# Optimization experiments

Measured on AMD Instinct MI355X. Metric: run time of the kernel, lower is better.

Reference implementation:

```python
import jax, jax.numpy as jnp
import numpy as np

H = 128; L = 4; B = 128; NPG = 32
N = B * NPG; E = B * NPG * NPG
NFREQ = 10; DIS = 2 * 3 * NFREQ; EIN = 2 * H + 9 + DIS  # 325


def setup_inputs() -> dict:
    key = jax.random.key(0)
    ks = jax.random.split(key, 16)
    atom_types = jax.random.randint(ks[0], (N,), 1, 101, dtype=jnp.int32)  # atomic numbers 1..100
    frac_coords = jax.random.uniform(ks[1], (N, 3), dtype=jnp.float32)
    lattices = jax.random.normal(ks[2], (B, 3, 3), dtype=jnp.float32)
    # fully-connected edges per graph incl. self-loops == block_diag(ones(n,n)) -> dense_to_sparse
    off = np.arange(B, dtype=np.int32)[:, None, None] * NPG
    rows = np.broadcast_to(np.arange(NPG, dtype=np.int32)[:, None], (NPG, NPG))
    cols = np.broadcast_to(np.arange(NPG, dtype=np.int32)[None, :], (NPG, NPG))
    edges = jnp.asarray(np.stack([(off + rows).reshape(E), (off + cols).reshape(E)]))
    node2graph = jnp.asarray(np.repeat(np.arange(B, dtype=np.int32), NPG))
    s = 0.02
    p = lambda k, shp: s * jax.random.normal(k, shp, dtype=jnp.float32)
    return dict(
        atom_types=atom_types, frac_coords=frac_coords, lattices=lattices,
        edges=edges, node2graph=node2graph,
        node_emb=p(ks[3], (100, H)),
        edge_w1=p(ks[4], (L, EIN, H)), edge_b1=jnp.zeros((L, H), jnp.float32),
        edge_w2=p(ks[5], (L, H, H)), edge_b2=jnp.zeros((L, H), jnp.float32),
        node_w1=p(ks[6], (L, 2 * H, H)), node_b1=jnp.zeros((L, H), jnp.float32),
        node_w2=p(ks[7], (L, H, H)), node_b2=jnp.zeros((L, H), jnp.float32),
        out_w=p(ks[8], (H, H)))


def _sin_emb(x):  # SinusoidsEmbedding: [E,3] -> [E, 2*3*NFREQ]
    freqs = 2.0 * jnp.pi * jnp.arange(NFREQ, dtype=x.dtype)
    e = (x[:, :, None] * freqs).reshape(x.shape[0], 3 * NFREQ)
    return jnp.concatenate([jnp.sin(e), jnp.cos(e)], axis=-1)


def reference(atom_types, frac_coords, lattices, edges, node2graph, node_emb,
              edge_w1, edge_b1, edge_w2, edge_b2,
              node_w1, node_b1, node_w2, node_b2, out_w):
    src, dst = edges[0], edges[1]
    frac_diff = frac_coords[dst] - frac_coords[src]            # gen_edges
    dis = jax.lax.stop_gradient(_sin_emb(frac_diff))           # dis_emb returns .detach()
    edge2graph = node2graph[src]
    lat_ip = jnp.einsum('bij,bkj->bik', lattices, lattices).reshape(-1, 9)  # ip=True
    lat_e = lat_ip[edge2graph]                                  # [E,9]
    h = node_emb[atom_types - 1]                                # [N,H]
    ones_e = jnp.ones((E,), h.dtype)
    cnt = jnp.clip(jax.ops.segment_sum(ones_e, src, num_segments=N), 1.0)[:, None]
    for l in range(L):  # CSPLayer, ln=False
        m = jnp.concatenate([h[src], h[dst], lat_e, dis], axis=-1)  # [E,325]
        m = jax.nn.silu(m @ edge_w1[l] + edge_b1[l])
        m = jax.nn.silu(m @ edge_w2[l] + edge_b2[l])                # edge features [E,H]
        agg = jax.ops.segment_sum(m, src, num_segments=N) / cnt     # scatter-mean onto edge_index[0]
        u = jnp.concatenate([h, agg], axis=-1)
        u = jax.nn.silu(u @ node_w1[l] + node_b1[l])
        u = jax.nn.silu(u @ node_w2[l] + node_b2[l])
        h = h + u                                                   # residual
    gcnt = jnp.clip(jax.ops.segment_sum(jnp.ones((N,), h.dtype), node2graph, num_segments=B), 1.0)[:, None]
    g = jax.ops.segment_sum(h, node2graph, num_segments=B) / gcnt   # scatter-mean pooling
    return g @ out_w                                                # out_node (no bias)
```

## Files before the change

kernel.cpp:

```cpp
#include <hip/hip_runtime.h>
#include <hip/hip_bf16.h>
#include <cstdint>

#define HH 128
#define LL 4
#define BB 128
#define NNODE 4096
#define EIN 325
#define NBLK 1024

#define OFF_W1  0
#define OFF_W2  80
#define OFF_NW1 112
#define OFF_NW2 176
#define FR_PER_L 208

typedef __attribute__((ext_vector_type(8))) short short8;
typedef __attribute__((ext_vector_type(4))) float float4v;

#define MFMA __builtin_amdgcn_mfma_f32_16x16x32_bf16

__device__ __forceinline__ float silu_f(float x) {
    return x / (1.0f + __expf(-x));
}

__device__ __forceinline__ uint16_t f2bf(float x) {
    uint32_t u = __builtin_bit_cast(uint32_t, x);
    u += 0x7FFFu + ((u >> 16) & 1u);
    return (uint16_t)(u >> 16);
}

__device__ __forceinline__ short8 ldw(const uint4* wpl, int fidx, int lane) {
    return *reinterpret_cast<const short8*>(&wpl[(size_t)fidx*64 + lane]);
}

__global__ __launch_bounds__(256) void k_prep(
    const int* __restrict__ at, const float* __restrict__ frac,
    const float* __restrict__ lat, const float* __restrict__ emb,
    const float* __restrict__ ew1, const float* __restrict__ eb1,
    const float* __restrict__ ew2, const float* __restrict__ nw1,
    const float* __restrict__ nw2,
    uint4* __restrict__ disP, uint4* __restrict__ wp,
    float* __restrict__ h0, float* __restrict__ Cc)
{
    __shared__ uint16_t sm[8192];
    int gid = blockIdx.x, t = threadIdx.x;

    if (gid < 1024) {
        #pragma unroll
        for (int z = 0; z < 4; ++z) ((uint4*)sm)[t + 256*z] = uint4{0,0,0,0};
        __syncthreads();
        int b = gid >> 3, q4 = gid & 7;
        int e2 = t >> 1, half = t & 1;
        int i = q4*4 + (e2 >> 5), j = e2 & 31;
        float dx[3];
        #pragma unroll
        for (int d = 0; d < 3; ++d)
            dx[d] = frac[(b*32 + j)*3 + d] - frac[(b*32 + i)*3 + d];
        int T = e2 >> 4, rr = e2 & 15;
        #pragma unroll
        for (int kk = 0; kk < 30; ++kk) {
            int d = kk / 10, f = kk % 10;
            float ang = 6.28318530717958647692f * (float)f * dx[d];
            float v = half ? __cosf(ang) : __sinf(ang);
            int k = kk + 30*half;
            int ks = k >> 5, g = (k >> 3) & 3, ii = k & 7;
            sm[((ks*8 + T)*64 + g*16 + rr)*8 + ii] = f2bf(v);
        }
        __syncthreads();
        uint4* dst = disP + (size_t)gid * 1024;
        const uint4* smv = (const uint4*)sm;
        #pragma unroll
        for (int z = 0; z < 4; ++z) dst[t + 256*z] = smv[t + 256*z];
    } else if (gid < 1128) {
        int jidx = gid - 1024;
        int lay = jidx / 26, jj = jidx % 26;
        int wv = t >> 6, lane = t & 63, g = lane >> 4, col = lane & 15;
        int ks, base, type;
        if (jj < 10)      { ks = jj;      base = OFF_W1;  type = 0; }
        else if (jj < 14) { ks = jj - 10; base = OFF_W2;  type = 1; }
        else if (jj < 22) { ks = jj - 14; base = OFF_NW1; type = 2; }
        else              { ks = jj - 22; base = OFF_NW2; type = 3; }
        for (int nn = 0; nn < 2; ++nn) {
            int nf = 2*wv + nn;
            int n = nf*16 + col;
            uint16_t vals[8];
            #pragma unroll
            for (int ii = 0; ii < 8; ++ii) {
                int gk = 32*ks + 8*g + ii;
                float v = 0.f;
                if (type == 0) {
                    if (gk < 256)       v = ew1[((size_t)lay*EIN + gk)*HH + n];
                    else if (gk < 316)  v = ew1[((size_t)lay*EIN + gk + 9)*HH + n];
                } else if (type == 1)   v = ew2[((size_t)lay*HH + gk)*HH + n];
                else if (type == 2)     v = nw1[((size_t)lay*2*HH + gk)*HH + n];
                else                    v = nw2[((size_t)lay*HH + gk)*HH + n];
                vals[ii] = f2bf(v);
            }
            wp[((size_t)lay*FR_PER_L + base + ks*8 + nf)*64 + lane] = *(const uint4*)vals;
        }
    } else if (gid < 1640) {
        float* lip = (float*)sm;
        int blk = gid - 1128;
        int lay = blk >> 7, b = blk & 127;
        if (t < 9) {
            int i = t / 3, k2 = t % 3;
            const float* lb = lat + b*9;
            lip[t] = lb[i*3]*lb[k2*3] + lb[i*3+1]*lb[k2*3+1] + lb[i*3+2]*lb[k2*3+2];
        }
        __syncthreads();
        if (t < 128) {
            float acc = eb1[lay*HH + t];
            #pragma unroll
            for (int k = 0; k < 9; ++k)
                acc += lip[k] * ew1[((size_t)lay*EIN + 2*HH + k)*HH + t];
            Cc[(size_t)blk*HH + t] = acc;
        }
    } else {
        int idx = (gid - 1640)*256 + t;
        int n = idx >> 5, cq = idx & 31;
        float4v v = *(const float4v*)&emb[((size_t)(at[n]-1))*HH + cq*4];
        *(float4v*)&h0[(size_t)n*HH + cq*4] = v;
    }
}

__global__ __launch_bounds__(256, 4) void k_layer(
    const float* __restrict__ h_in, float* __restrict__ h_out,
    const uint4* __restrict__ disP, const uint4* __restrict__ wpl,
    const float* __restrict__ Cc_l, const float* __restrict__ b2,
    const float* __restrict__ nb1, const float* __restrict__ nb2)
{
    __shared__ uint4 smem4[2560];
    char* smem = (char*)smem4;
    char* hHi = smem;
    float* Af = (float*)(smem + 8192);
    float* Bf = (float*)(smem + 10304);
    char* sS  = smem + 8192;

    int bid = blockIdx.x;
    int b = bid >> 3, q4 = bid & 7;
    uint16_t* aggB = (uint16_t*)(smem + ((((q4 + 1) & 7)) << 10));
    uint16_t* u1B  = (uint16_t*)(smem + ((((q4 + 2) & 7)) << 10));
    int t = threadIdx.x;
    int w = t >> 6, l = t & 63;
    int wm = w >> 1, wn = w & 1;
    int g = l >> 4, rr = l & 15;

    short8 dfr[2][4];
    #pragma unroll
    for (int ks = 0; ks < 2; ++ks)
        #pragma unroll
        for (int mf = 0; mf < 4; ++mf)
            dfr[ks][mf] = *(const short8*)&disP[((size_t)(bid*2 + ks)*8 + 4*wm + mf)*64 + l];

    {
        int row = t >> 3, czb = (t & 7) * 16;
        const float* hp = h_in + (size_t)(b*32 + row)*HH + czb;
        uint16_t ph[16];
        #pragma unroll
        for (int z = 0; z < 16; z += 4) {
            float4v v = *(const float4v*)(hp + z);
            #pragma unroll
            for (int y = 0; y < 4; ++y) ph[z+y] = f2bf(v[y]);
        }
        int sw = (row & 7) << 4;
        int base = row * 256;
        *(uint4*)(hHi + base + ((2*czb) ^ sw))      = *(const uint4*)&ph[0];
        *(uint4*)(hHi + base + ((2*czb + 16) ^ sw)) = *(const uint4*)&ph[8];
    }
    __syncthreads();

    {
        float4v pacc[3][2];
        #pragma unroll
        for (int mt = 0; mt < 3; ++mt)
            #pragma unroll
            for (int nfl = 0; nfl < 2; ++nfl) pacc[mt][nfl] = (float4v){0.f,0.f,0.f,0.f};
        #pragma unroll
        for (int ks = 0; ks < 4; ++ks) {
            short8 wa[2], wb[2];
            #pragma unroll
            for (int nfl = 0; nfl < 2; ++nfl) {
                wa[nfl] = ldw(wpl, OFF_W1      + ks*8 + 2*w + nfl, l);
                wb[nfl] = ldw(wpl, OFF_W1 + 32 + ks*8 + 2*w + nfl, l);
            }
            #pragma unroll
            for (int mt = 0; mt < 3; ++mt) {
                int R = (mt == 0) ? (q4*4 + (rr & 3)) : ((mt - 1)*16 + rr);
                short8 a = *(const short8*)(hHi + R*256 + ((64*ks + 16*g) ^ ((R & 7) << 4)));
                #pragma unroll
                for (int nfl = 0; nfl < 2; ++nfl)
                    pacc[mt][nfl] = MFMA(a, (mt == 0) ? wa[nfl] : wb[nfl], pacc[mt][nfl], 0, 0, 0);
            }
        }
        #pragma unroll
        for (int nfl = 0; nfl < 2; ++nfl) {
            int n = 32*w + 16*nfl + rr;
            if (g == 0) {
                #pragma unroll
                for (int r = 0; r < 4; ++r) Af[r*132 + n] = pacc[0][nfl][r];
            }
            #pragma unroll
            for (int r = 0; r < 4; ++r) Bf[(4*g + r)*132 + n]      = pacc[1][nfl][r];
            #pragma unroll
            for (int r = 0; r < 4; ++r) Bf[(16 + 4*g + r)*132 + n] = pacc[2][nfl][r];
        }
    }
    __syncthreads();

    float ccv[4], b2v[4];
    #pragma unroll
    for (int nf = 0; nf < 4; ++nf) {
        ccv[nf] = Cc_l[b*HH + 64*wn + 16*nf + rr];
        b2v[nf] = b2[64*wn + 16*nf + rr];
    }

    float4v acc[4][4];
    #pragma unroll
    for (int mf = 0; mf < 4; ++mf) {
        int srcr = 2*wm + (mf >> 1);
        #pragma unroll
        for (int nf = 0; nf < 4; ++nf) {
            float iv = ccv[nf] + Af[srcr*132 + 64*wn + 16*nf + rr];
            acc[mf][nf] = (float4v){iv, iv, iv, iv};
        }
    }
    #pragma unroll
    for (int ks = 0; ks < 2; ++ks) {
        short8 wf[4];
        #pragma unroll
        for (int nf = 0; nf < 4; ++nf)
            wf[nf] = ldw(wpl, OFF_W1 + 64 + ks*8 + 4*wn + nf, l);
        #pragma unroll
        for (int mf = 0; mf < 4; ++mf)
            #pragma unroll
            for (int nf = 0; nf < 4; ++nf)
                acc[mf][nf] = MFMA(dfr[ks][mf], wf[nf], acc[mf][nf], 0, 0, 0);
    }
    #pragma unroll
    for (int mf = 0; mf < 4; ++mf)
        #pragma unroll
        for (int r = 0; r < 4; ++r) {
            const float* bp = &Bf[(16*(mf & 1) + 4*g + r)*132 + 64*wn + rr];
            #pragma unroll
            for (int nf = 0; nf < 4; ++nf)
                acc[mf][nf][r] += bp[16*nf];
        }
    __syncthreads();

    #pragma unroll
    for (int mf = 0; mf < 4; ++mf) {
        int T = 4*wm + mf;
        #pragma unroll
        for (int nf = 0; nf < 4; ++nf) {
            int n = 64*wn + 16*nf + rr;
            #pragma unroll
            for (int r = 0; r < 4; ++r) {
                int m = 16*T + 4*g + r;
                *(uint16_t*)(sS + m*256 + ((2*n) ^ ((m & 7) << 4))) = f2bf(silu_f(acc[mf][nf][r]));
            }
        }
    }
    __syncthreads();

    #pragma unroll
    for (int mf = 0; mf < 4; ++mf)
        #pragma unroll
        for (int nf = 0; nf < 4; ++nf)
            acc[mf][nf] = (float4v){0.f, 0.f, 0.f, 0.f};
    #pragma unroll
    for (int ks = 0; ks < 4; ++ks) {
        short8 wf[4];
        #pragma unroll
        for (int nf = 0; nf < 4; ++nf)
            wf[nf] = ldw(wpl, OFF_W2 + ks*8 + 4*wn + nf, l);
        #pragma unroll
        for (int mf = 0; mf < 4; ++mf) {
            int m = 16*(4*wm + mf) + rr;
            short8 a = *(const short8*)(sS + m*256 + ((64*ks + 16*g) ^ ((m & 7) << 4)));
            #pragma unroll
            for (int nf = 0; nf < 4; ++nf)
                acc[mf][nf] = MFMA(a, wf[nf], acc[mf][nf], 0, 0, 0);
        }
    }

    #pragma unroll
    for (int u = 0; u < 2; ++u) {
        #pragma unroll
        for (int nf = 0; nf < 4; ++nf) {
            float v = 0.f;
            #pragma unroll
            for (int mm = 0; mm < 2; ++mm)
                #pragma unroll
                for (int r = 0; r < 4; ++r)
                    v += silu_f(acc[2*u + mm][nf][r] + b2v[nf]);
            v += __shfl_xor(v, 16);
            v += __shfl_xor(v, 32);
            if (g == 0)
                aggB[(2*wm + u)*128 + 64*wn + 16*nf + rr] = f2bf(v * (1.0f/32.0f));
        }
    }
    __syncthreads();

    float4v uacc[2];
    #pragma unroll
    for (int nfl = 0; nfl < 2; ++nfl) uacc[nfl] = (float4v){0.f, 0.f, 0.f, 0.f};
    #pragma unroll
    for (int ks = 0; ks < 8; ++ks) {
        short8 a;
        if (ks < 4) {
            int R = q4*4 + (rr & 3);
            a = *(const short8*)(hHi + R*256 + ((64*ks + 16*g) ^ ((R & 7) << 4)));
        } else {
            a = *(const short8*)&aggB[(rr & 3)*128 + 32*(ks - 4) + 8*g];
        }
        #pragma unroll
        for (int nfl = 0; nfl < 2; ++nfl)
            uacc[nfl] = MFMA(a, ldw(wpl, OFF_NW1 + ks*8 + 2*w + nfl, l), uacc[nfl], 0, 0, 0);
    }
    if (g == 0) {
        #pragma unroll
        for (int nfl = 0; nfl < 2; ++nfl)
            #pragma unroll
            for (int r = 0; r < 4; ++r) {
                int col = (2*w + nfl)*16 + rr;
                u1B[r*128 + col] = f2bf(silu_f(uacc[nfl][r] + nb1[col]));
            }
    }
    __syncthreads();

    float4v vacc[2];
    #pragma unroll
    for (int nfl = 0; nfl < 2; ++nfl) vacc[nfl] = (float4v){0.f, 0.f, 0.f, 0.f};
    #pragma unroll
    for (int ks = 0; ks < 4; ++ks) {
        short8 a = *(const short8*)&u1B[(rr & 3)*128 + 32*ks + 8*g];
        #pragma unroll
        for (int nfl = 0; nfl < 2; ++nfl)
            vacc[nfl] = MFMA(a, ldw(wpl, OFF_NW2 + ks*8 + 2*w + nfl, l), vacc[nfl], 0, 0, 0);
    }
    if (g == 0) {
        #pragma unroll
        for (int nfl = 0; nfl < 2; ++nfl)
            #pragma unroll
            for (int r = 0; r < 4; ++r) {
                int col = (2*w + nfl)*16 + rr;
                size_t node = (size_t)(b*32 + q4*4 + r);
                h_out[node*HH + col] = h_in[node*HH + col] + silu_f(vacc[nfl][r] + nb2[col]);
            }
    }
}

__global__ __launch_bounds__(128) void k_pool(const float* __restrict__ h, const float* __restrict__ ow,
                       float* __restrict__ out) {
    __shared__ float sm_g[HH];
    int b = blockIdx.x, c = threadIdx.x;
    float s = 0.f;
    for (int n = 0; n < 32; ++n) s += h[(size_t)(b*32 + n)*HH + c];
    sm_g[c] = s * (1.0f/32.0f);
    __syncthreads();
    float acc = 0.f;
    for (int k = 0; k < HH; ++k) acc += sm_g[k] * ow[k*HH + c];
    out[(size_t)b*HH + c] = acc;
}

extern "C" void kernel_launch(void* const* d_in, const int* in_sizes, int n_in,
                              void* d_out, int out_size, void* d_ws, size_t ws_size,
                              hipStream_t stream) {
    const int*   atom_types = (const int*)d_in[0];
    const float* frac       = (const float*)d_in[1];
    const float* lat        = (const float*)d_in[2];
    const float* node_emb   = (const float*)d_in[5];
    const float* ew1        = (const float*)d_in[6];
    const float* eb1        = (const float*)d_in[7];
    const float* ew2        = (const float*)d_in[8];
    const float* eb2        = (const float*)d_in[9];
    const float* nw1        = (const float*)d_in[10];
    const float* nb1        = (const float*)d_in[11];
    const float* nw2        = (const float*)d_in[12];
    const float* nb2        = (const float*)d_in[13];
    const float* ow         = (const float*)d_in[14];
    float* out = (float*)d_out;

    char* ws = (char*)d_ws;
    uint4* disP = (uint4*)ws; ws += (size_t)NBLK*1024*16;
    uint4* wp   = (uint4*)ws; ws += (size_t)LL*FR_PER_L*64*16;
    float* hA   = (float*)ws; ws += (size_t)NNODE*HH*4;
    float* hB   = (float*)ws; ws += (size_t)NNODE*HH*4;
    float* Cc   = (float*)ws; ws += (size_t)LL*BB*HH*4;

    k_prep<<<2152, 256, 0, stream>>>(atom_types, frac, lat, node_emb,
                                     ew1, eb1, ew2, nw1, nw2,
                                     disP, wp, hA, Cc);

    float* hin = hA; float* hout = hB;
    for (int l = 0; l < LL; ++l) {
        k_layer<<<NBLK, 256, 0, stream>>>(hin, hout, disP, wp + (size_t)l*FR_PER_L*64,
                                          Cc + (size_t)l*BB*HH, eb2 + (size_t)l*HH,
                                          nb1 + (size_t)l*HH, nb2 + (size_t)l*HH);
        float* tmp = hin; hin = hout; hout = tmp;
    }
    k_pool<<<BB, HH, 0, stream>>>(hin, ow, out);
}
```

Baseline: 229.6 us.

## Double waves per layer block and use hardware bf16 pack and exp/rcp SiLU

```diff
diff --git a/kernel.cpp b/kernel.cpp
--- a/kernel.cpp
+++ b/kernel.cpp
@@ -20,14 +20,19 @@
 
 #define MFMA __builtin_amdgcn_mfma_f32_16x16x32_bf16
 
+__device__ __forceinline__ uint32_t cvtpk2(float lo, float hi) {
+    uint32_t r;
+    asm("v_cvt_pk_bf16_f32 %0, %1, %2" : "=v"(r) : "v"(lo), "v"(hi));
+    return r;
+}
+__device__ __forceinline__ uint16_t f2bf(float x) { return (uint16_t)cvtpk2(x, x); }
+
 __device__ __forceinline__ float silu_f(float x) {
-    return x / (1.0f + __expf(-x));
-}
-
-__device__ __forceinline__ uint16_t f2bf(float x) {
-    uint32_t u = __builtin_bit_cast(uint32_t, x);
-    u += 0x7FFFu + ((u >> 16) & 1u);
-    return (uint16_t)(u >> 16);
+    float e;
+    asm("v_exp_f32 %0, %1" : "=v"(e) : "v"(-1.44269504088896341f * x));
+    float r;
+    asm("v_rcp_f32 %0, %1" : "=v"(r) : "v"(1.0f + e));
+    return x * r;
 }
 
 __device__ __forceinline__ short8 ldw(const uint4* wpl, int fidx, int lane) {
@@ -124,7 +129,7 @@
     }
 }
 
-__global__ __launch_bounds__(256, 4) void k_layer(
+__global__ __launch_bounds__(512, 4) void k_layer(
     const float* __restrict__ h_in, float* __restrict__ h_out,
     const uint4* __restrict__ disP, const uint4* __restrict__ wpl,
     const float* __restrict__ Cc_l, const float* __restrict__ b2,
@@ -143,7 +148,7 @@
     uint16_t* u1B  = (uint16_t*)(smem + ((((q4 + 2) & 7)) << 10));
     int t = threadIdx.x;
     int w = t >> 6, l = t & 63;
-    int wm = w >> 1, wn = w & 1;
+    int wm = w >> 2, wn = w & 3;
     int g = l >> 4, rr = l & 15;
 
     short8 dfr[2][4];
@@ -154,96 +159,80 @@
             dfr[ks][mf] = *(const short8*)&disP[((size_t)(bid*2 + ks)*8 + 4*wm + mf)*64 + l];
 
     {
-        int row = t >> 3, czb = (t & 7) * 16;
-        const float* hp = h_in + (size_t)(b*32 + row)*HH + czb;
-        uint16_t ph[16];
-        #pragma unroll
-        for (int z = 0; z < 16; z += 4) {
-            float4v v = *(const float4v*)(hp + z);
-            #pragma unroll
-            for (int y = 0; y < 4; ++y) ph[z+y] = f2bf(v[y]);
-        }
-        int sw = (row & 7) << 4;
-        int base = row * 256;
-        *(uint4*)(hHi + base + ((2*czb) ^ sw))      = *(const uint4*)&ph[0];
-        *(uint4*)(hHi + base + ((2*czb + 16) ^ sw)) = *(const uint4*)&ph[8];
+        int row = t >> 4, cz = (t & 15) * 8;
+        const float* hp = h_in + (size_t)(b*32 + row)*HH + cz;
+        float4v v0 = *(const float4v*)hp;
+        float4v v1 = *(const float4v*)(hp + 4);
+        uint32_t pw[4];
+        pw[0] = cvtpk2(v0[0], v0[1]); pw[1] = cvtpk2(v0[2], v0[3]);
+        pw[2] = cvtpk2(v1[0], v1[1]); pw[3] = cvtpk2(v1[2], v1[3]);
+        *(uint4*)(hHi + row*256 + ((2*cz) ^ ((row & 7) << 4))) = *(const uint4*)pw;
     }
     __syncthreads();
 
     {
-        float4v pacc[3][2];
-        #pragma unroll
-        for (int mt = 0; mt < 3; ++mt)
-            #pragma unroll
-            for (int nfl = 0; nfl < 2; ++nfl) pacc[mt][nfl] = (float4v){0.f,0.f,0.f,0.f};
+        float4v pacc[3];
+        #pragma unroll
+        for (int mt = 0; mt < 3; ++mt) pacc[mt] = (float4v){0.f,0.f,0.f,0.f};
         #pragma unroll
         for (int ks = 0; ks < 4; ++ks) {
-            short8 wa[2], wb[2];
-            #pragma unroll
-            for (int nfl = 0; nfl < 2; ++nfl) {
-                wa[nfl] = ldw(wpl, OFF_W1      + ks*8 + 2*w + nfl, l);
-                wb[nfl] = ldw(wpl, OFF_W1 + 32 + ks*8 + 2*w + nfl, l);
-            }
+            short8 wa = ldw(wpl, OFF_W1      + ks*8 + w, l);
+            short8 wb = ldw(wpl, OFF_W1 + 32 + ks*8 + w, l);
             #pragma unroll
             for (int mt = 0; mt < 3; ++mt) {
                 int R = (mt == 0) ? (q4*4 + (rr & 3)) : ((mt - 1)*16 + rr);
                 short8 a = *(const short8*)(hHi + R*256 + ((64*ks + 16*g) ^ ((R & 7) << 4)));
-                #pragma unroll
-                for (int nfl = 0; nfl < 2; ++nfl)
-                    pacc[mt][nfl] = MFMA(a, (mt == 0) ? wa[nfl] : wb[nfl], pacc[mt][nfl], 0, 0, 0);
+                pacc[mt] = MFMA(a, (mt == 0) ? wa : wb, pacc[mt], 0, 0, 0);
             }
         }
-        #pragma unroll
-        for (int nfl = 0; nfl < 2; ++nfl) {
-            int n = 32*w + 16*nfl + rr;
-            if (g == 0) {
-                #pragma unroll
-                for (int r = 0; r < 4; ++r) Af[r*132 + n] = pacc[0][nfl][r];
-            }
-            #pragma unroll
-            for (int r = 0; r < 4; ++r) Bf[(4*g + r)*132 + n]      = pacc[1][nfl][r];
-            #pragma unroll
-            for (int r = 0; r < 4; ++r) Bf[(16 + 4*g + r)*132 + n] = pacc[2][nfl][r];
-        }
-    }
-    __syncthreads();
-
-    float ccv[4], b2v[4];
-    #pragma unroll
-    for (int nf = 0; nf < 4; ++nf) {
-        ccv[nf] = Cc_l[b*HH + 64*wn + 16*nf + rr];
-        b2v[nf] = b2[64*wn + 16*nf + rr];
-    }
-
-    float4v acc[4][4];
+        int n = 16*w + rr;
+        if (g == 0) {
+            #pragma unroll
+            for (int r = 0; r < 4; ++r) Af[r*132 + n] = pacc[0][r];
+        }
+        #pragma unroll
+        for (int r = 0; r < 4; ++r) Bf[(4*g + r)*132 + n]      = pacc[1][r];
+        #pragma unroll
+        for (int r = 0; r < 4; ++r) Bf[(16 + 4*g + r)*132 + n] = pacc[2][r];
+    }
+    __syncthreads();
+
+    float ccv[2], b2v[2];
+    #pragma unroll
+    for (int nf = 0; nf < 2; ++nf) {
+        ccv[nf] = Cc_l[b*HH + 32*wn + 16*nf + rr];
+        b2v[nf] = b2[32*wn + 16*nf + rr];
+    }
+
+    float4v acc[4][2];
     #pragma unroll
     for (int mf = 0; mf < 4; ++mf) {
         int srcr = 2*wm + (mf >> 1);
         #pragma unroll
-        for (int nf = 0; nf < 4; ++nf) {
-            float iv = ccv[nf] + Af[srcr*132 + 64*wn + 16*nf + rr];
+        for (int nf = 0; nf < 2; ++nf) {
+            float iv = ccv[nf] + Af[srcr*132 + 32*wn + 16*nf + rr];
             acc[mf][nf] = (float4v){iv, iv, iv, iv};
         }
     }
     #pragma unroll
     for (int ks = 0; ks < 2; ++ks) {
-        short8 wf[4];
-        #pragma unroll
-        for (int nf = 0; nf < 4; ++nf)
-            wf[nf] = ldw(wpl, OFF_W1 + 64 + ks*8 + 4*wn + nf, l);
+        short8 wf[2];
+        #pragma unroll
+        for (int nf = 0; nf < 2; ++nf)
+            wf[nf] = ldw(wpl, OFF_W1 + 64 + ks*8 + 2*wn + nf, l);
         #pragma unroll
         for (int mf = 0; mf < 4; ++mf)
             #pragma unroll
-            for (int nf = 0; nf < 4; ++nf)
+            for (int nf = 0; nf < 2; ++nf)
                 acc[mf][nf] = MFMA(dfr[ks][mf], wf[nf], acc[mf][nf], 0, 0, 0);
     }
     #pragma unroll
     for (int mf = 0; mf < 4; ++mf)
         #pragma unroll
         for (int r = 0; r < 4; ++r) {
-            const float* bp = &Bf[(16*(mf & 1) + 4*g + r)*132 + 64*wn + rr];
-            #pragma unroll
-            for (int nf = 0; nf < 4; ++nf)
+            const float* bp = &Bf[(16*(mf & 1) + 4*g + r)*132 + 32*wn + rr];
+            #pragma unroll
+            for (int nf = 0; nf < 2; ++nf)
                 acc[mf][nf][r] += bp[16*nf];
         }
     __syncthreads();
@@ -252,8 +241,8 @@
     for (int mf = 0; mf < 4; ++mf) {
         int T = 4*wm + mf;
         #pragma unroll
-        for (int nf = 0; nf < 4; ++nf) {
-            int n = 64*wn + 16*nf + rr;
+        for (int nf = 0; nf < 2; ++nf) {
+            int n = 32*wn + 16*nf + rr;
             #pragma unroll
             for (int r = 0; r < 4; ++r) {
                 int m = 16*T + 4*g + r;
@@ -266,20 +255,20 @@
     #pragma unroll
     for (int mf = 0; mf < 4; ++mf)
         #pragma unroll
-        for (int nf = 0; nf < 4; ++nf)
+        for (int nf = 0; nf < 2; ++nf)
             acc[mf][nf] = (float4v){0.f, 0.f, 0.f, 0.f};
     #pragma unroll
     for (int ks = 0; ks < 4; ++ks) {
-        short8 wf[4];
-        #pragma unroll
-        for (int nf = 0; nf < 4; ++nf)
-            wf[nf] = ldw(wpl, OFF_W2 + ks*8 + 4*wn + nf, l);
+        short8 wf[2];
+        #pragma unroll
+        for (int nf = 0; nf < 2; ++nf)
+            wf[nf] = ldw(wpl, OFF_W2 + ks*8 + 2*wn + nf, l);
         #pragma unroll
         for (int mf = 0; mf < 4; ++mf) {
             int m = 16*(4*wm + mf) + rr;
             short8 a = *(const short8*)(sS + m*256 + ((64*ks + 16*g) ^ ((m & 7) << 4)));
             #pragma unroll
-            for (int nf = 0; nf < 4; ++nf)
+            for (int nf = 0; nf < 2; ++nf)
                 acc[mf][nf] = MFMA(a, wf[nf], acc[mf][nf], 0, 0, 0);
         }
     }
@@ -287,7 +276,7 @@
     #pragma unroll
     for (int u = 0; u < 2; ++u) {
         #pragma unroll
-        for (int nf = 0; nf < 4; ++nf) {
+        for (int nf = 0; nf < 2; ++nf) {
             float v = 0.f;
             #pragma unroll
             for (int mm = 0; mm < 2; ++mm)
@@ -297,14 +286,12 @@
             v += __shfl_xor(v, 16);
             v += __shfl_xor(v, 32);
             if (g == 0)
-                aggB[(2*wm + u)*128 + 64*wn + 16*nf + rr] = f2bf(v * (1.0f/32.0f));
-        }
-    }
-    __syncthreads();
-
-    float4v uacc[2];
-    #pragma unroll
-    for (int nfl = 0; nfl < 2; ++nfl) uacc[nfl] = (float4v){0.f, 0.f, 0.f, 0.f};
+                aggB[(2*wm + u)*128 + 32*wn + 16*nf + rr] = f2bf(v * (1.0f/32.0f));
+        }
+    }
+    __syncthreads();
+
+    float4v uacc = (float4v){0.f, 0.f, 0.f, 0.f};
     #pragma unroll
     for (int ks = 0; ks < 8; ++ks) {
         short8 a;
@@ -314,40 +301,30 @@
         } else {
             a = *(const short8*)&aggB[(rr & 3)*128 + 32*(ks - 4) + 8*g];
         }
-        #pragma unroll
-        for (int nfl = 0; nfl < 2; ++nfl)
-            uacc[nfl] = MFMA(a, ldw(wpl, OFF_NW1 + ks*8 + 2*w + nfl, l), uacc[nfl], 0, 0, 0);
+        uacc = MFMA(a, ldw(wpl, OFF_NW1 + ks*8 + w, l), uacc, 0, 0, 0);
     }
     if (g == 0) {
         #pragma unroll
-        for (int nfl = 0; nfl < 2; ++nfl)
-            #pragma unroll
-            for (int r = 0; r < 4; ++r) {
-                int col = (2*w + nfl)*16 + rr;
-                u1B[r*128 + col] = f2bf(silu_f(uacc[nfl][r] + nb1[col]));
-            }
-    }
-    __syncthreads();
-
-    float4v vacc[2];
-    #pragma unroll
-    for (int nfl = 0; nfl < 2; ++nfl) vacc[nfl] = (float4v){0.f, 0.f, 0.f, 0.f};
+        for (int r = 0; r < 4; ++r) {
+            int col = 16*w + rr;
+            u1B[r*128 + col] = f2bf(silu_f(uacc[r] + nb1[col]));
+        }
+    }
+    __syncthreads();
+
+    float4v vacc = (float4v){0.f, 0.f, 0.f, 0.f};
     #pragma unroll
     for (int ks = 0; ks < 4; ++ks) {
         short8 a = *(const short8*)&u1B[(rr & 3)*128 + 32*ks + 8*g];
-        #pragma unroll
-        for (int nfl = 0; nfl < 2; ++nfl)
-            vacc[nfl] = MFMA(a, ldw(wpl, OFF_NW2 + ks*8 + 2*w + nfl, l), vacc[nfl], 0, 0, 0);
+        vacc = MFMA(a, ldw(wpl, OFF_NW2 + ks*8 + w, l), vacc, 0, 0, 0);
     }
     if (g == 0) {
         #pragma unroll
-        for (int nfl = 0; nfl < 2; ++nfl)
-            #pragma unroll
-            for (int r = 0; r < 4; ++r) {
-                int col = (2*w + nfl)*16 + rr;
-                size_t node = (size_t)(b*32 + q4*4 + r);
-                h_out[node*HH + col] = h_in[node*HH + col] + silu_f(vacc[nfl][r] + nb2[col]);
-            }
+        for (int r = 0; r < 4; ++r) {
+            int col = 16*w + rr;
+            size_t node = (size_t)(b*32 + q4*4 + r);
+            h_out[node*HH + col] = h_in[node*HH + col] + silu_f(vacc[r] + nb2[col]);
+        }
     }
 }
 
@@ -395,7 +372,7 @@
 
     float* hin = hA; float* hout = hB;
     for (int l = 0; l < LL; ++l) {
-        k_layer<<<NBLK, 256, 0, stream>>>(hin, hout, disP, wp + (size_t)l*FR_PER_L*64,
+        k_layer<<<NBLK, 512, 0, stream>>>(hin, hout, disP, wp + (size_t)l*FR_PER_L*64,
                                           Cc + (size_t)l*BB*HH, eb2 + (size_t)l*HH,
                                           nb1 + (size_t)l*HH, nb2 + (size_t)l*HH);
         float* tmp = hin; hin = hout; hout = tmp;
```

Result: faster. 192.3 us (-16.2%).
